# Optimization experiments

Measured on AMD Instinct MI355X. Metric: run time of the kernel, lower is better.

## Reference

```python
import jax, jax.numpy as jnp
import numpy as np

N_NODES = 100000
N_EDGES = 1600000
H, D, DE = 4, 32, 32  # heads, node_out_feats, edge_out_feats
NEG_SLOPE = 0.2


def setup_inputs() -> dict:
    key = jax.random.key(0)
    ks = jax.random.split(key, 10)
    return {
        "node_inputs": jax.random.normal(ks[0], (N_NODES, 128), jnp.float32),
        "edge_inputs": jax.random.normal(ks[1], (N_EDGES, 16), jnp.float32),
        "src": jax.random.randint(ks[2], (N_EDGES,), 0, N_NODES, jnp.int32),
        "dst": jax.random.randint(ks[3], (N_EDGES,), 0, N_NODES, jnp.int32),
        "W_fc": jax.random.normal(ks[4], (128, H * D), jnp.float32) * 0.1,
        "attn_src_p": jax.random.normal(ks[5], (1, H, D), jnp.float32) * 0.1,
        "attn_dst_p": jax.random.normal(ks[6], (1, H, D), jnp.float32) * 0.1,
        "W_edge": jax.random.normal(ks[7], (16, H * DE), jnp.float32) * 0.1,
        "attn_edge_p": jax.random.normal(ks[8], (1, H, DE), jnp.float32) * 0.1,
        "W_res": jax.random.normal(ks[9], (128, H * D), jnp.float32) * 0.1,
        "bias_p": jnp.zeros((H * D,), jnp.float32),
    }


def reference(node_inputs, edge_inputs, src, dst, W_fc, attn_src_p,
              attn_dst_p, W_edge, attn_edge_p, W_res, bias_p):
    N = node_inputs.shape[0]
    # node projection: [N, H, D]
    feat = (node_inputs @ W_fc).reshape(N, H, D)
    # per-node attention logits [N, H]
    a_src = (feat * attn_src_p).sum(-1)
    a_dst = (feat * attn_dst_p).sum(-1)
    # edge-feature attention logits [E, H]
    feat_e = (edge_inputs @ W_edge).reshape(-1, H, DE)
    a_edge = (feat_e * attn_edge_p).sum(-1)
    # per-edge score: u_add_v + edge term, then LeakyReLU
    e = a_src[src] + a_dst[dst] + a_edge                 # [E, H]
    e = jnp.where(e > 0, e, NEG_SLOPE * e)
    # edge softmax grouped by destination node
    emax = jax.lax.stop_gradient(jax.ops.segment_max(e, dst, num_segments=N))
    ex = jnp.exp(e - emax[dst])
    denom = jax.ops.segment_sum(ex, dst, num_segments=N)
    attn = ex / denom[dst]                               # [E, H]
    # weighted scatter-aggregate of source features
    msg = feat[src] * attn[:, :, None]                   # [E, H, D]
    x = jax.ops.segment_sum(msg, dst, num_segments=N)    # [N, H, D]
    # residual + bias
    x = x + (node_inputs @ W_res).reshape(N, H, D)
    x = x + bias_p.reshape(H, D)
    return x
```

## Files before the change

kernel.cpp:

```cpp
#include <hip/hip_runtime.h>
#include <math.h>

#define NNODES_FEAT 128
#define HD 128
#define H 4
#define D 32
#define EDGE_F 16
#define NEG_SLOPE 0.2f

typedef _Float16 f16;
typedef _Float16 f16x2 __attribute__((ext_vector_type(2)));
typedef _Float16 f16x4 __attribute__((ext_vector_type(4)));
typedef _Float16 f16x8 __attribute__((ext_vector_type(8)));
typedef float f32x4 __attribute__((ext_vector_type(4)));

union ExPack { float2 f; f16x4 h; };

__global__ void k_wedge(const float* __restrict__ W_edge,
                        const float* __restrict__ attn_edge,
                        float* __restrict__ w_eh) {
    int t = threadIdx.x;
    int k = t >> 2;
    int h = t & 3;
    float s = 0.f;
    for (int d = 0; d < D; ++d)
        s += W_edge[k * HD + h * D + d] * attn_edge[h * D + d];
    w_eh[k * H + h] = s;
}

__global__ __launch_bounds__(256) void k_wt(const float* __restrict__ Wfc,
                                            const float* __restrict__ Wres,
                                            f16* __restrict__ Wt) {
    int i = blockIdx.x * 256 + threadIdx.x;
    int n = i >> 7, k = i & 127;
    float v = (n < 128) ? Wfc[k * HD + n] : Wres[k * HD + (n - 128)];
    Wt[(size_t)n * 128 + k] = (f16)v;
}

#define LDK 136
__global__ __launch_bounds__(256) void k_gemm_mfma(
    const float* __restrict__ A, const f16* __restrict__ Wt,
    const float* __restrict__ bias, f16* __restrict__ feat16,
    float* __restrict__ out, int N) {
    __shared__ f16 As[64 * LDK];
    __shared__ f16 Bs[128 * LDK];
    int tid = threadIdx.x;
    int wave = tid >> 6, lane = tid & 63;
    int m0 = blockIdx.x * 64;
    int cb = blockIdx.y;

    for (int c = tid; c < 64 * 32; c += 256) {
        int r = c >> 5, cc = (c & 31) * 4;
        int gr = m0 + r;
        float4 v = make_float4(0.f, 0.f, 0.f, 0.f);
        if (gr < N) v = *(const float4*)(A + (size_t)gr * 128 + cc);
        f16x4 h = {(f16)v.x, (f16)v.y, (f16)v.z, (f16)v.w};
        *(f16x4*)(&As[r * LDK + cc]) = h;
    }
    const f16* Wblk = Wt + (size_t)cb * 128 * 128;
    for (int c = tid; c < 128 * 16; c += 256) {
        int r = c >> 4, cc = (c & 15) * 8;
        float4 v = *(const float4*)(Wblk + (size_t)r * 128 + cc);
        *(float4*)(&Bs[r * LDK + cc]) = v;
    }
    __syncthreads();

    int am = lane & 15, aq = lane >> 4;
    f32x4 acc[8];
#pragma unroll
    for (int nt = 0; nt < 8; ++nt) acc[nt] = (f32x4){0.f, 0.f, 0.f, 0.f};

    int arow = wave * 16 + am;
#pragma unroll
    for (int kc = 0; kc < 4; ++kc) {
        f16x8 a = *(const f16x8*)(&As[arow * LDK + kc * 32 + aq * 8]);
#pragma unroll
        for (int nt = 0; nt < 8; ++nt) {
            f16x8 b = *(const f16x8*)(&Bs[(nt * 16 + am) * LDK + kc * 32 + aq * 8]);
            acc[nt] = __builtin_amdgcn_mfma_f32_16x16x32_f16(a, b, acc[nt], 0, 0, 0);
        }
    }

    int orow0 = m0 + wave * 16 + aq * 4;
    if (cb == 0) {
#pragma unroll
        for (int nt = 0; nt < 8; ++nt) {
            int col = nt * 16 + am;
#pragma unroll
            for (int r = 0; r < 4; ++r) {
                int row = orow0 + r;
                if (row < N) feat16[(size_t)row * 128 + col] = (f16)acc[nt][r];
            }
        }
    } else {
#pragma unroll
        for (int nt = 0; nt < 8; ++nt) {
            int col = nt * 16 + am;
            float bv = bias[col];
#pragma unroll
            for (int r = 0; r < 4; ++r) {
                int row = orow0 + r;
                if (row < N) out[(size_t)row * 128 + col] = acc[nt][r] + bv;
            }
        }
    }
}

__global__ __launch_bounds__(256) void k_attn_nodes(
    const f16* __restrict__ feat16, const float* __restrict__ attn_src,
    const float* __restrict__ attn_dst, float* __restrict__ a_src,
    float* __restrict__ a_dst, int N) {
    int g = blockIdx.x * 256 + threadIdx.x;
    int n = g >> 2, h = g & 3;
    if (n >= N) return;
    const f16* f = feat16 + (size_t)n * HD + h * D;
    const float* w1 = attn_src + h * D;
    const float* w2 = attn_dst + h * D;
    float s1 = 0.f, s2 = 0.f;
#pragma unroll
    for (int d = 0; d < D; d += 2) {
        f16x2 fv = *(const f16x2*)(f + d);
        float f0 = (float)fv.x, f1 = (float)fv.y;
        s1 += f0 * w1[d] + f1 * w1[d + 1];
        s2 += f0 * w2[d] + f1 * w2[d + 1];
    }
    a_src[n * H + h] = s1;
    a_dst[n * H + h] = s2;
}

__global__ __launch_bounds__(256) void k_count(const int* __restrict__ dst,
                                               int* __restrict__ deg, int E) {
    int e = blockIdx.x * 256 + threadIdx.x;
    if (e < E) atomicAdd(deg + dst[e], 1);
}

__global__ __launch_bounds__(256) void k_scan_partial(
    const int* __restrict__ deg, int* __restrict__ partial, int N) {
    __shared__ int sdata[256];
    int t = threadIdx.x;
    int base = blockIdx.x * 1024 + t * 4;
    int s = 0;
#pragma unroll
    for (int j = 0; j < 4; ++j) { int i = base + j; if (i < N) s += deg[i]; }
    sdata[t] = s;
    __syncthreads();
    for (int off = 128; off > 0; off >>= 1) {
        if (t < off) sdata[t] += sdata[t + off];
        __syncthreads();
    }
    if (t == 0) partial[blockIdx.x] = sdata[0];
}

__global__ __launch_bounds__(256) void k_scan_top(
    int* __restrict__ partial, int* __restrict__ offs, int nb, int N) {
    __shared__ int sdata[256];
    int t = threadIdx.x;
    int v = (t < nb) ? partial[t] : 0;
    sdata[t] = v;
    __syncthreads();
    for (int off = 1; off < 256; off <<= 1) {
        int add = (t >= off) ? sdata[t - off] : 0;
        __syncthreads();
        sdata[t] += add;
        __syncthreads();
    }
    int excl = (t == 0) ? 0 : sdata[t - 1];
    if (t < nb) partial[t] = excl;
    if (t == nb - 1) offs[N] = sdata[t];
}

__global__ __launch_bounds__(256) void k_scan_final(
    int* __restrict__ deg_offs, const int* __restrict__ partial,
    int* __restrict__ cursor, int N) {
    __shared__ int sdata[256];
    int t = threadIdx.x;
    int base = blockIdx.x * 1024 + t * 4;
    int v[4]; int s = 0;
#pragma unroll
    for (int j = 0; j < 4; ++j) { int i = base + j; v[j] = (i < N) ? deg_offs[i] : 0; s += v[j]; }
    sdata[t] = s;
    __syncthreads();
    for (int off = 1; off < 256; off <<= 1) {
        int add = (t >= off) ? sdata[t - off] : 0;
        __syncthreads();
        sdata[t] += add;
        __syncthreads();
    }
    int excl = partial[blockIdx.x] + ((t == 0) ? 0 : sdata[t - 1]);
#pragma unroll
    for (int j = 0; j < 4; ++j) {
        int i = base + j;
        if (i < N) { deg_offs[i] = excl; cursor[i] = excl; excl += v[j]; }
    }
}

__global__ __launch_bounds__(256) void k_edge_fill(
    const float* __restrict__ edge_inputs, const int* __restrict__ src,
    const int* __restrict__ dst, const float* __restrict__ w_eh,
    const float* __restrict__ a_src, const float* __restrict__ a_dst,
    int* __restrict__ cursor, float4* __restrict__ rec, int E) {
    __shared__ float weh_s[EDGE_F * H];
    if (threadIdx.x < EDGE_F * H) weh_s[threadIdx.x] = w_eh[threadIdx.x];
    __syncthreads();

    int base = blockIdx.x * 512 + threadIdx.x;
#pragma unroll
    for (int j = 0; j < 2; ++j) {
        int e = base + j * 256;
        if (e >= E) continue;

        const float* x = edge_inputs + (long)e * EDGE_F;
        float ae[H] = {0.f, 0.f, 0.f, 0.f};
#pragma unroll
        for (int k = 0; k < EDGE_F; ++k) {
            float xv = x[k];
#pragma unroll
            for (int h = 0; h < H; ++h) ae[h] += xv * weh_s[k * H + h];
        }
        int s = src[e], d = dst[e];
        float4 as = *(const float4*)(a_src + s * H);
        float4 ad = *(const float4*)(a_dst + d * H);
        float ev[H];
        ev[0] = as.x + ad.x + ae[0];
        ev[1] = as.y + ad.y + ae[1];
        ev[2] = as.z + ad.z + ae[2];
        ev[3] = as.w + ad.w + ae[3];
#pragma unroll
        for (int h = 0; h < H; ++h) {
            float t = ev[h];
            t = t > 0.f ? t : NEG_SLOPE * t;
            ev[h] = __expf(t);
        }
        int pos = atomicAdd(cursor + d, 1);
        ExPack p;
        p.h = (f16x4){(f16)ev[0], (f16)ev[1], (f16)ev[2], (f16)ev[3]};
        float4 r;
        r.x = __int_as_float(s);
        r.y = p.f.x;
        r.z = p.f.y;
        r.w = 0.f;
        rec[pos] = r;
    }
}

__global__ __launch_bounds__(256) void k_aggr(
    const f16* __restrict__ feat16, const float4* __restrict__ rec,
    const int* __restrict__ offs, float* __restrict__ out, int N) {
    int wave = threadIdx.x >> 6;
    int lane = threadIdx.x & 63;
    int n = blockIdx.x * 4 + wave;
    if (n >= N) return;
    int beg = offs[n], end = offs[n + 1];
    if (end <= beg) return;
    int h = lane >> 4;
    size_t c0 = (size_t)2 * lane;
    float num0 = 0.f, num1 = 0.f, den = 0.f;
    int i = beg;
    for (; i + 3 < end; i += 4) {
        float4 r0 = rec[i], r1 = rec[i + 1], r2 = rec[i + 2], r3 = rec[i + 3];
        int s0 = __float_as_int(r0.x), s1 = __float_as_int(r1.x);
        int s2 = __float_as_int(r2.x), s3 = __float_as_int(r3.x);
        f16x2 f0 = *(const f16x2*)(feat16 + (size_t)s0 * HD + c0);
        f16x2 f1 = *(const f16x2*)(feat16 + (size_t)s1 * HD + c0);
        f16x2 f2 = *(const f16x2*)(feat16 + (size_t)s2 * HD + c0);
        f16x2 f3 = *(const f16x2*)(feat16 + (size_t)s3 * HD + c0);
        ExPack p0, p1, p2, p3;
        p0.f = make_float2(r0.y, r0.z);
        p1.f = make_float2(r1.y, r1.z);
        p2.f = make_float2(r2.y, r2.z);
        p3.f = make_float2(r3.y, r3.z);
        float e0 = (float)p0.h[h], e1 = (float)p1.h[h];
        float e2 = (float)p2.h[h], e3 = (float)p3.h[h];
        num0 += e0 * (float)f0.x + e1 * (float)f1.x + e2 * (float)f2.x + e3 * (float)f3.x;
        num1 += e0 * (float)f0.y + e1 * (float)f1.y + e2 * (float)f2.y + e3 * (float)f3.y;
        den += e0 + e1 + e2 + e3;
    }
    for (; i < end; ++i) {
        float4 r0 = rec[i];
        int s0 = __float_as_int(r0.x);
        f16x2 f0 = *(const f16x2*)(feat16 + (size_t)s0 * HD + c0);
        ExPack p0;
        p0.f = make_float2(r0.y, r0.z);
        float e0 = (float)p0.h[h];
        num0 += e0 * (float)f0.x;
        num1 += e0 * (float)f0.y;
        den += e0;
    }
    float inv = 1.f / den;
    size_t o = (size_t)n * HD + c0;
    float2 v = *(float2*)(out + o);
    v.x += num0 * inv;
    v.y += num1 * inv;
    *(float2*)(out + o) = v;
}

extern "C" void kernel_launch(void* const* d_in, const int* in_sizes, int n_in,
                              void* d_out, int out_size, void* d_ws, size_t ws_size,
                              hipStream_t stream) {
    const float* node_inputs = (const float*)d_in[0];
    const float* edge_inputs = (const float*)d_in[1];
    const int*   src         = (const int*)d_in[2];
    const int*   dst         = (const int*)d_in[3];
    const float* W_fc        = (const float*)d_in[4];
    const float* attn_src_p  = (const float*)d_in[5];
    const float* attn_dst_p  = (const float*)d_in[6];
    const float* W_edge      = (const float*)d_in[7];
    const float* attn_edge_p = (const float*)d_in[8];
    const float* W_res       = (const float*)d_in[9];
    const float* bias_p      = (const float*)d_in[10];

    int N = in_sizes[0] / NNODES_FEAT;
    int E = in_sizes[2];

    float* out = (float*)d_out;

    f16*    feat16  = (f16*)d_ws;
    float4* rec     = (float4*)(feat16 + (size_t)N * HD);
    f16*    Wt      = (f16*)(rec + (size_t)E);
    float*  a_src   = (float*)(Wt + 256 * 128);
    float*  a_dst   = a_src + (size_t)N * H;
    float*  w_eh    = a_dst + (size_t)N * H;
    int*    deg     = (int*)(w_eh + 64);
    int*    offs    = deg;
    int*    cursor  = deg + (N + 2);
    int*    partial = cursor + N;

    hipMemsetAsync(deg, 0, (size_t)(N + 2) * sizeof(int), stream);

    k_wedge<<<1, 64, 0, stream>>>(W_edge, attn_edge_p, w_eh);
    k_wt<<<(256 * 128) / 256, 256, 0, stream>>>(W_fc, W_res, Wt);

    dim3 g1((N + 63) / 64, 2);
    k_gemm_mfma<<<g1, 256, 0, stream>>>(node_inputs, Wt, bias_p, feat16, out, N);

    int nb = (N * H + 255) / 256;
    k_attn_nodes<<<nb, 256, 0, stream>>>(feat16, attn_src_p, attn_dst_p, a_src, a_dst, N);

    int eb = (E + 255) / 256;
    k_count<<<eb, 256, 0, stream>>>(dst, deg, E);
    int sb = (N + 1023) / 1024;
    k_scan_partial<<<sb, 256, 0, stream>>>(deg, partial, N);
    k_scan_top<<<1, 256, 0, stream>>>(partial, offs, sb, N);
    k_scan_final<<<sb, 256, 0, stream>>>(deg, partial, cursor, N);

    int eb2 = (E + 511) / 512;
    k_edge_fill<<<eb2, 256, 0, stream>>>(edge_inputs, src, dst, w_eh, a_src, a_dst,
                                         cursor, rec, E);

    int ab = (N + 3) / 4;
    k_aggr<<<ab, 256, 0, stream>>>(feat16, rec, offs, out, N);
}
```

Baseline: 516.3 us.

## Write edge records in edge order and sort via an index permutation

The edge-score kernel now writes each edge record to its original edge slot and counts degree in the same pass, which removes the separate count kernel. A new lightweight kernel scatters edge indices into CSR order using the cursors. Aggregation reads the records indirectly through this index. Record writes become coalesced, at the cost of one extra scatter pass and a random 16-byte gather per edge in aggregation.

```diff
diff --git a/kernel.cpp b/kernel.cpp
--- a/kernel.cpp
+++ b/kernel.cpp
@@ -128,77 +128,11 @@
     a_dst[n * H + h] = s2;
 }
 
-__global__ __launch_bounds__(256) void k_count(const int* __restrict__ dst,
-                                               int* __restrict__ deg, int E) {
-    int e = blockIdx.x * 256 + threadIdx.x;
-    if (e < E) atomicAdd(deg + dst[e], 1);
-}
-
-__global__ __launch_bounds__(256) void k_scan_partial(
-    const int* __restrict__ deg, int* __restrict__ partial, int N) {
-    __shared__ int sdata[256];
-    int t = threadIdx.x;
-    int base = blockIdx.x * 1024 + t * 4;
-    int s = 0;
-#pragma unroll
-    for (int j = 0; j < 4; ++j) { int i = base + j; if (i < N) s += deg[i]; }
-    sdata[t] = s;
-    __syncthreads();
-    for (int off = 128; off > 0; off >>= 1) {
-        if (t < off) sdata[t] += sdata[t + off];
-        __syncthreads();
-    }
-    if (t == 0) partial[blockIdx.x] = sdata[0];
-}
-
-__global__ __launch_bounds__(256) void k_scan_top(
-    int* __restrict__ partial, int* __restrict__ offs, int nb, int N) {
-    __shared__ int sdata[256];
-    int t = threadIdx.x;
-    int v = (t < nb) ? partial[t] : 0;
-    sdata[t] = v;
-    __syncthreads();
-    for (int off = 1; off < 256; off <<= 1) {
-        int add = (t >= off) ? sdata[t - off] : 0;
-        __syncthreads();
-        sdata[t] += add;
-        __syncthreads();
-    }
-    int excl = (t == 0) ? 0 : sdata[t - 1];
-    if (t < nb) partial[t] = excl;
-    if (t == nb - 1) offs[N] = sdata[t];
-}
-
-__global__ __launch_bounds__(256) void k_scan_final(
-    int* __restrict__ deg_offs, const int* __restrict__ partial,
-    int* __restrict__ cursor, int N) {
-    __shared__ int sdata[256];
-    int t = threadIdx.x;
-    int base = blockIdx.x * 1024 + t * 4;
-    int v[4]; int s = 0;
-#pragma unroll
-    for (int j = 0; j < 4; ++j) { int i = base + j; v[j] = (i < N) ? deg_offs[i] : 0; s += v[j]; }
-    sdata[t] = s;
-    __syncthreads();
-    for (int off = 1; off < 256; off <<= 1) {
-        int add = (t >= off) ? sdata[t - off] : 0;
-        __syncthreads();
-        sdata[t] += add;
-        __syncthreads();
-    }
-    int excl = partial[blockIdx.x] + ((t == 0) ? 0 : sdata[t - 1]);
-#pragma unroll
-    for (int j = 0; j < 4; ++j) {
-        int i = base + j;
-        if (i < N) { deg_offs[i] = excl; cursor[i] = excl; excl += v[j]; }
-    }
-}
-
-__global__ __launch_bounds__(256) void k_edge_fill(
+__global__ __launch_bounds__(256) void k_fill_count(
     const float* __restrict__ edge_inputs, const int* __restrict__ src,
     const int* __restrict__ dst, const float* __restrict__ w_eh,
     const float* __restrict__ a_src, const float* __restrict__ a_dst,
-    int* __restrict__ cursor, float4* __restrict__ rec, int E) {
+    int* __restrict__ deg, float4* __restrict__ recE, int E) {
     __shared__ float weh_s[EDGE_F * H];
     if (threadIdx.x < EDGE_F * H) weh_s[threadIdx.x] = w_eh[threadIdx.x];
     __syncthreads();
@@ -231,7 +165,6 @@
             t = t > 0.f ? t : NEG_SLOPE * t;
             ev[h] = __expf(t);
         }
-        int pos = atomicAdd(cursor + d, 1);
         ExPack p;
         p.h = (f16x4){(f16)ev[0], (f16)ev[1], (f16)ev[2], (f16)ev[3]};
         float4 r;
@@ -239,13 +172,90 @@
         r.y = p.f.x;
         r.z = p.f.y;
         r.w = 0.f;
-        rec[pos] = r;
+        recE[e] = r;
+        atomicAdd(deg + d, 1);
+    }
+}
+
+__global__ __launch_bounds__(256) void k_scan_partial(
+    const int* __restrict__ deg, int* __restrict__ partial, int N) {
+    __shared__ int sdata[256];
+    int t = threadIdx.x;
+    int base = blockIdx.x * 1024 + t * 4;
+    int s = 0;
+#pragma unroll
+    for (int j = 0; j < 4; ++j) { int i = base + j; if (i < N) s += deg[i]; }
+    sdata[t] = s;
+    __syncthreads();
+    for (int off = 128; off > 0; off >>= 1) {
+        if (t < off) sdata[t] += sdata[t + off];
+        __syncthreads();
+    }
+    if (t == 0) partial[blockIdx.x] = sdata[0];
+}
+
+__global__ __launch_bounds__(256) void k_scan_top(
+    int* __restrict__ partial, int* __restrict__ offs, int nb, int N) {
+    __shared__ int sdata[256];
+    int t = threadIdx.x;
+    int v = (t < nb) ? partial[t] : 0;
+    sdata[t] = v;
+    __syncthreads();
+    for (int off = 1; off < 256; off <<= 1) {
+        int add = (t >= off) ? sdata[t - off] : 0;
+        __syncthreads();
+        sdata[t] += add;
+        __syncthreads();
+    }
+    int excl = (t == 0) ? 0 : sdata[t - 1];
+    if (t < nb) partial[t] = excl;
+    if (t == nb - 1) offs[N] = sdata[t];
+}
+
+__global__ __launch_bounds__(256) void k_scan_final(
+    int* __restrict__ deg_offs, const int* __restrict__ partial,
+    int* __restrict__ cursor, int N) {
+    __shared__ int sdata[256];
+    int t = threadIdx.x;
+    int base = blockIdx.x * 1024 + t * 4;
+    int v[4]; int s = 0;
+#pragma unroll
+    for (int j = 0; j < 4; ++j) { int i = base + j; v[j] = (i < N) ? deg_offs[i] : 0; s += v[j]; }
+    sdata[t] = s;
+    __syncthreads();
+    for (int off = 1; off < 256; off <<= 1) {
+        int add = (t >= off) ? sdata[t - off] : 0;
+        __syncthreads();
+        sdata[t] += add;
+        __syncthreads();
+    }
+    int excl = partial[blockIdx.x] + ((t == 0) ? 0 : sdata[t - 1]);
+#pragma unroll
+    for (int j = 0; j < 4; ++j) {
+        int i = base + j;
+        if (i < N) { deg_offs[i] = excl; cursor[i] = excl; excl += v[j]; }
+    }
+}
+
+__global__ __launch_bounds__(256) void k_perm(
+    const int* __restrict__ dst, int* __restrict__ cursor,
+    int* __restrict__ eidx, int E) {
+    int base = blockIdx.x * 2048 + threadIdx.x;
+#pragma unroll
+    for (int j = 0; j < 8; ++j) {
+        int e = base + j * 256;
+        if (e < E) {
+            int d = dst[e];
+            int pos = atomicAdd(cursor + d, 1);
+            eidx[pos] = e;
+        }
     }
 }
 
 __global__ __launch_bounds__(256) void k_aggr(
-    const f16* __restrict__ feat16, const float4* __restrict__ rec,
-    const int* __restrict__ offs, float* __restrict__ out, int N) {
+    const f16* __restrict__ feat16, const float4* __restrict__ recE,
+    const int* __restrict__ eidx, const int* __restrict__ offs,
+    float* __restrict__ out, int N) {
     int wave = threadIdx.x >> 6;
     int lane = threadIdx.x & 63;
     int n = blockIdx.x * 4 + wave;
@@ -257,7 +267,8 @@
     float num0 = 0.f, num1 = 0.f, den = 0.f;
     int i = beg;
     for (; i + 3 < end; i += 4) {
-        float4 r0 = rec[i], r1 = rec[i + 1], r2 = rec[i + 2], r3 = rec[i + 3];
+        int e0 = eidx[i], e1 = eidx[i + 1], e2 = eidx[i + 2], e3 = eidx[i + 3];
+        float4 r0 = recE[e0], r1 = recE[e1], r2 = recE[e2], r3 = recE[e3];
         int s0 = __float_as_int(r0.x), s1 = __float_as_int(r1.x);
         int s2 = __float_as_int(r2.x), s3 = __float_as_int(r3.x);
         f16x2 f0 = *(const f16x2*)(feat16 + (size_t)s0 * HD + c0);
@@ -269,22 +280,23 @@
         p1.f = make_float2(r1.y, r1.z);
         p2.f = make_float2(r2.y, r2.z);
         p3.f = make_float2(r3.y, r3.z);
-        float e0 = (float)p0.h[h], e1 = (float)p1.h[h];
-        float e2 = (float)p2.h[h], e3 = (float)p3.h[h];
-        num0 += e0 * (float)f0.x + e1 * (float)f1.x + e2 * (float)f2.x + e3 * (float)f3.x;
-        num1 += e0 * (float)f0.y + e1 * (float)f1.y + e2 * (float)f2.y + e3 * (float)f3.y;
-        den += e0 + e1 + e2 + e3;
+        float e0v = (float)p0.h[h], e1v = (float)p1.h[h];
+        float e2v = (float)p2.h[h], e3v = (float)p3.h[h];
+        num0 += e0v * (float)f0.x + e1v * (float)f1.x + e2v * (float)f2.x + e3v * (float)f3.x;
+        num1 += e0v * (float)f0.y + e1v * (float)f1.y + e2v * (float)f2.y + e3v * (float)f3.y;
+        den += e0v + e1v + e2v + e3v;
     }
     for (; i < end; ++i) {
-        float4 r0 = rec[i];
+        int e0 = eidx[i];
+        float4 r0 = recE[e0];
         int s0 = __float_as_int(r0.x);
         f16x2 f0 = *(const f16x2*)(feat16 + (size_t)s0 * HD + c0);
         ExPack p0;
         p0.f = make_float2(r0.y, r0.z);
-        float e0 = (float)p0.h[h];
-        num0 += e0 * (float)f0.x;
-        num1 += e0 * (float)f0.y;
-        den += e0;
+        float e0v = (float)p0.h[h];
+        num0 += e0v * (float)f0.x;
+        num1 += e0v * (float)f0.y;
+        den += e0v;
     }
     float inv = 1.f / den;
     size_t o = (size_t)n * HD + c0;
@@ -315,8 +327,9 @@
     float* out = (float*)d_out;
 
     f16*    feat16  = (f16*)d_ws;
-    float4* rec     = (float4*)(feat16 + (size_t)N * HD);
-    f16*    Wt      = (f16*)(rec + (size_t)E);
+    float4* recE    = (float4*)(feat16 + (size_t)N * HD);
+    int*    eidx    = (int*)(recE + (size_t)E);
+    f16*    Wt      = (f16*)(eidx + (size_t)E);
     float*  a_src   = (float*)(Wt + 256 * 128);
     float*  a_dst   = a_src + (size_t)N * H;
     float*  w_eh    = a_dst + (size_t)N * H;
@@ -336,17 +349,18 @@
     int nb = (N * H + 255) / 256;
     k_attn_nodes<<<nb, 256, 0, stream>>>(feat16, attn_src_p, attn_dst_p, a_src, a_dst, N);
 
-    int eb = (E + 255) / 256;
-    k_count<<<eb, 256, 0, stream>>>(dst, deg, E);
+    int eb2 = (E + 511) / 512;
+    k_fill_count<<<eb2, 256, 0, stream>>>(edge_inputs, src, dst, w_eh, a_src, a_dst,
+                                          deg, recE, E);
+
     int sb = (N + 1023) / 1024;
     k_scan_partial<<<sb, 256, 0, stream>>>(deg, partial, N);
     k_scan_top<<<1, 256, 0, stream>>>(partial, offs, sb, N);
     k_scan_final<<<sb, 256, 0, stream>>>(deg, partial, cursor, N);
 
-    int eb2 = (E + 511) / 512;
-    k_edge_fill<<<eb2, 256, 0, stream>>>(edge_inputs, src, dst, w_eh, a_src, a_dst,
-                                         cursor, rec, E);
+    int pb = (E + 2047) / 2048;
+    k_perm<<<pb, 256, 0, stream>>>(dst, cursor, eidx, E);
 
     int ab = (N + 3) / 4;
-    k_aggr<<<ab, 256, 0, stream>>>(feat16, rec, offs, out, N);
-}
+    k_aggr<<<ab, 256, 0, stream>>>(feat16, recE, eidx, offs, out, N);
+}
```

After: 603.4 us. 1.17x slower.

## Replace global-atomic CSR scatter with two-level bucketed partition sort

Applied to the files above, without the earlier changes.

Edge scores are now written in original edge order, and degree counting is fused into that fill kernel along with a per-bucket histogram. A coarse pass partitions edge indices into 196 destination buckets, and a fine pass per bucket scatters records into CSR order using shared-memory cursors. This replaces random global atomicAdd cursors and scattered 16-byte writes with more local writes. The cost is extra passes, a 16-byte-per-edge record buffer and an index buffer, plus bucket-count constants that assume N is at most 196*512.

```diff
diff --git a/kernel.cpp b/kernel.cpp
--- a/kernel.cpp
+++ b/kernel.cpp
@@ -7,6 +7,10 @@
 #define D 32
 #define EDGE_F 16
 #define NEG_SLOPE 0.2f
+
+#define CB_SHIFT 9
+#define NBUCK 196
+#define BH_STRIDE 16
 
 typedef _Float16 f16;
 typedef _Float16 f16x2 __attribute__((ext_vector_type(2)));
@@ -128,79 +132,16 @@
     a_dst[n * H + h] = s2;
 }
 
-__global__ __launch_bounds__(256) void k_count(const int* __restrict__ dst,
-                                               int* __restrict__ deg, int E) {
-    int e = blockIdx.x * 256 + threadIdx.x;
-    if (e < E) atomicAdd(deg + dst[e], 1);
-}
-
-__global__ __launch_bounds__(256) void k_scan_partial(
-    const int* __restrict__ deg, int* __restrict__ partial, int N) {
-    __shared__ int sdata[256];
-    int t = threadIdx.x;
-    int base = blockIdx.x * 1024 + t * 4;
-    int s = 0;
-#pragma unroll
-    for (int j = 0; j < 4; ++j) { int i = base + j; if (i < N) s += deg[i]; }
-    sdata[t] = s;
-    __syncthreads();
-    for (int off = 128; off > 0; off >>= 1) {
-        if (t < off) sdata[t] += sdata[t + off];
-        __syncthreads();
-    }
-    if (t == 0) partial[blockIdx.x] = sdata[0];
-}
-
-__global__ __launch_bounds__(256) void k_scan_top(
-    int* __restrict__ partial, int* __restrict__ offs, int nb, int N) {
-    __shared__ int sdata[256];
-    int t = threadIdx.x;
-    int v = (t < nb) ? partial[t] : 0;
-    sdata[t] = v;
-    __syncthreads();
-    for (int off = 1; off < 256; off <<= 1) {
-        int add = (t >= off) ? sdata[t - off] : 0;
-        __syncthreads();
-        sdata[t] += add;
-        __syncthreads();
-    }
-    int excl = (t == 0) ? 0 : sdata[t - 1];
-    if (t < nb) partial[t] = excl;
-    if (t == nb - 1) offs[N] = sdata[t];
-}
-
-__global__ __launch_bounds__(256) void k_scan_final(
-    int* __restrict__ deg_offs, const int* __restrict__ partial,
-    int* __restrict__ cursor, int N) {
-    __shared__ int sdata[256];
-    int t = threadIdx.x;
-    int base = blockIdx.x * 1024 + t * 4;
-    int v[4]; int s = 0;
-#pragma unroll
-    for (int j = 0; j < 4; ++j) { int i = base + j; v[j] = (i < N) ? deg_offs[i] : 0; s += v[j]; }
-    sdata[t] = s;
-    __syncthreads();
-    for (int off = 1; off < 256; off <<= 1) {
-        int add = (t >= off) ? sdata[t - off] : 0;
-        __syncthreads();
-        sdata[t] += add;
-        __syncthreads();
-    }
-    int excl = partial[blockIdx.x] + ((t == 0) ? 0 : sdata[t - 1]);
-#pragma unroll
-    for (int j = 0; j < 4; ++j) {
-        int i = base + j;
-        if (i < N) { deg_offs[i] = excl; cursor[i] = excl; excl += v[j]; }
-    }
-}
-
-__global__ __launch_bounds__(256) void k_edge_fill(
+__global__ __launch_bounds__(256) void k_fill_count(
     const float* __restrict__ edge_inputs, const int* __restrict__ src,
     const int* __restrict__ dst, const float* __restrict__ w_eh,
     const float* __restrict__ a_src, const float* __restrict__ a_dst,
-    int* __restrict__ cursor, float4* __restrict__ rec, int E) {
+    int* __restrict__ deg, int* __restrict__ bhist,
+    float4* __restrict__ recE, int E) {
     __shared__ float weh_s[EDGE_F * H];
+    __shared__ int hist[NBUCK];
     if (threadIdx.x < EDGE_F * H) weh_s[threadIdx.x] = w_eh[threadIdx.x];
+    if (threadIdx.x < NBUCK) hist[threadIdx.x] = 0;
     __syncthreads();
 
     int base = blockIdx.x * 512 + threadIdx.x;
@@ -231,7 +172,6 @@
             t = t > 0.f ? t : NEG_SLOPE * t;
             ev[h] = __expf(t);
         }
-        int pos = atomicAdd(cursor + d, 1);
         ExPack p;
         p.h = (f16x4){(f16)ev[0], (f16)ev[1], (f16)ev[2], (f16)ev[3]};
         float4 r;
@@ -239,7 +179,145 @@
         r.y = p.f.x;
         r.z = p.f.y;
         r.w = 0.f;
-        rec[pos] = r;
+        recE[e] = r;
+        atomicAdd(deg + d, 1);
+        atomicAdd(&hist[d >> CB_SHIFT], 1);
+    }
+    __syncthreads();
+    if (threadIdx.x < NBUCK && hist[threadIdx.x] > 0)
+        atomicAdd(bhist + threadIdx.x * BH_STRIDE, hist[threadIdx.x]);
+}
+
+__global__ __launch_bounds__(256) void k_scan_partial(
+    const int* __restrict__ deg, int* __restrict__ partial, int N) {
+    __shared__ int sdata[256];
+    int t = threadIdx.x;
+    int base = blockIdx.x * 1024 + t * 4;
+    int s = 0;
+#pragma unroll
+    for (int j = 0; j < 4; ++j) { int i = base + j; if (i < N) s += deg[i]; }
+    sdata[t] = s;
+    __syncthreads();
+    for (int off = 128; off > 0; off >>= 1) {
+        if (t < off) sdata[t] += sdata[t + off];
+        __syncthreads();
+    }
+    if (t == 0) partial[blockIdx.x] = sdata[0];
+}
+
+__global__ __launch_bounds__(256) void k_scan_top(
+    int* __restrict__ partial, int* __restrict__ offs, int nb, int N) {
+    __shared__ int sdata[256];
+    int t = threadIdx.x;
+    int v = (t < nb) ? partial[t] : 0;
+    sdata[t] = v;
+    __syncthreads();
+    for (int off = 1; off < 256; off <<= 1) {
+        int add = (t >= off) ? sdata[t - off] : 0;
+        __syncthreads();
+        sdata[t] += add;
+        __syncthreads();
+    }
+    int excl = (t == 0) ? 0 : sdata[t - 1];
+    if (t < nb) partial[t] = excl;
+    if (t == nb - 1) offs[N] = sdata[t];
+}
+
+__global__ __launch_bounds__(256) void k_scan_final(
+    int* __restrict__ deg_offs, const int* __restrict__ partial, int N) {
+    __shared__ int sdata[256];
+    int t = threadIdx.x;
+    int base = blockIdx.x * 1024 + t * 4;
+    int v[4]; int s = 0;
+#pragma unroll
+    for (int j = 0; j < 4; ++j) { int i = base + j; v[j] = (i < N) ? deg_offs[i] : 0; s += v[j]; }
+    sdata[t] = s;
+    __syncthreads();
+    for (int off = 1; off < 256; off <<= 1) {
+        int add = (t >= off) ? sdata[t - off] : 0;
+        __syncthreads();
+        sdata[t] += add;
+        __syncthreads();
+    }
+    int excl = partial[blockIdx.x] + ((t == 0) ? 0 : sdata[t - 1]);
+#pragma unroll
+    for (int j = 0; j < 4; ++j) {
+        int i = base + j;
+        if (i < N) { deg_offs[i] = excl; excl += v[j]; }
+    }
+}
+
+__global__ __launch_bounds__(256) void k_bscan(
+    const int* __restrict__ bhist, int* __restrict__ bbase,
+    int* __restrict__ gcur) {
+    __shared__ int sdata[256];
+    int t = threadIdx.x;
+    int v = (t < NBUCK) ? bhist[t * BH_STRIDE] : 0;
+    sdata[t] = v;
+    __syncthreads();
+    for (int off = 1; off < 256; off <<= 1) {
+        int add = (t >= off) ? sdata[t - off] : 0;
+        __syncthreads();
+        sdata[t] += add;
+        __syncthreads();
+    }
+    int excl = (t == 0) ? 0 : sdata[t - 1];
+    if (t < NBUCK) {
+        bbase[t] = excl;
+        gcur[t * BH_STRIDE] = excl;
+    }
+    if (t == NBUCK - 1) bbase[NBUCK] = sdata[t];
+}
+
+__global__ __launch_bounds__(256) void k_part_coarse(
+    const int* __restrict__ dst, int* __restrict__ gcur,
+    int* __restrict__ ebuck, int E) {
+    __shared__ int hist[NBUCK];
+    __shared__ int curl[NBUCK];
+    int t = threadIdx.x;
+    if (t < NBUCK) hist[t] = 0;
+    __syncthreads();
+
+    int base = blockIdx.x * 4096;
+#pragma unroll
+    for (int j = 0; j < 16; ++j) {
+        int e = base + j * 256 + t;
+        if (e < E) atomicAdd(&hist[dst[e] >> CB_SHIFT], 1);
+    }
+    __syncthreads();
+    if (t < NBUCK && hist[t] > 0)
+        curl[t] = atomicAdd(&gcur[t * BH_STRIDE], hist[t]);
+    __syncthreads();
+#pragma unroll
+    for (int j = 0; j < 16; ++j) {
+        int e = base + j * 256 + t;
+        if (e < E) {
+            int b = dst[e] >> CB_SHIFT;
+            int pos = atomicAdd(&curl[b], 1);
+            ebuck[pos] = e;
+        }
+    }
+}
+
+__global__ __launch_bounds__(1024) void k_part_fine(
+    const int* __restrict__ dst, const int* __restrict__ ebuck,
+    const int* __restrict__ bbase, const int* __restrict__ offs,
+    const float4* __restrict__ recE, float4* __restrict__ rec_sorted, int N) {
+    __shared__ int cur[1 << CB_SHIFT];
+    int t = threadIdx.x;
+    int b = blockIdx.x;
+    int dbase = b << CB_SHIFT;
+    if (t < (1 << CB_SHIFT)) {
+        int idx = dbase + t;
+        cur[t] = offs[idx < N ? idx : N];
+    }
+    __syncthreads();
+    int beg = bbase[b], end = bbase[b + 1];
+    for (int i = beg + t; i < end; i += 1024) {
+        int e = ebuck[i];
+        int d = dst[e];
+        int pos = atomicAdd(&cur[d - dbase], 1);
+        rec_sorted[pos] = recE[e];
     }
 }
 
@@ -314,18 +392,22 @@
 
     float* out = (float*)d_out;
 
-    f16*    feat16  = (f16*)d_ws;
-    float4* rec     = (float4*)(feat16 + (size_t)N * HD);
-    f16*    Wt      = (f16*)(rec + (size_t)E);
-    float*  a_src   = (float*)(Wt + 256 * 128);
-    float*  a_dst   = a_src + (size_t)N * H;
-    float*  w_eh    = a_dst + (size_t)N * H;
-    int*    deg     = (int*)(w_eh + 64);
-    int*    offs    = deg;
-    int*    cursor  = deg + (N + 2);
-    int*    partial = cursor + N;
-
-    hipMemsetAsync(deg, 0, (size_t)(N + 2) * sizeof(int), stream);
+    f16*    feat16     = (f16*)d_ws;
+    float4* recE       = (float4*)(feat16 + (size_t)N * HD);
+    float4* rec_sorted = recE + (size_t)E;
+    int*    ebuck      = (int*)(rec_sorted + (size_t)E);
+    f16*    Wt         = (f16*)(ebuck + (size_t)E);
+    float*  a_src      = (float*)(Wt + 256 * 128);
+    float*  a_dst      = a_src + (size_t)N * H;
+    float*  w_eh       = a_dst + (size_t)N * H;
+    int*    deg        = (int*)(w_eh + 64);
+    int*    offs       = deg;
+    int*    bhist      = deg + (N + 2);
+    int*    gcur       = bhist + NBUCK * BH_STRIDE;
+    int*    bbase      = gcur + NBUCK * BH_STRIDE;
+    int*    partial    = bbase + (NBUCK + 4);
+
+    hipMemsetAsync(deg, 0, (size_t)(N + 2 + NBUCK * BH_STRIDE) * sizeof(int), stream);
 
     k_wedge<<<1, 64, 0, stream>>>(W_edge, attn_edge_p, w_eh);
     k_wt<<<(256 * 128) / 256, 256, 0, stream>>>(W_fc, W_res, Wt);
@@ -336,17 +418,21 @@
     int nb = (N * H + 255) / 256;
     k_attn_nodes<<<nb, 256, 0, stream>>>(feat16, attn_src_p, attn_dst_p, a_src, a_dst, N);
 
-    int eb = (E + 255) / 256;
-    k_count<<<eb, 256, 0, stream>>>(dst, deg, E);
+    int eb2 = (E + 511) / 512;
+    k_fill_count<<<eb2, 256, 0, stream>>>(edge_inputs, src, dst, w_eh, a_src, a_dst,
+                                          deg, bhist, recE, E);
+
     int sb = (N + 1023) / 1024;
     k_scan_partial<<<sb, 256, 0, stream>>>(deg, partial, N);
     k_scan_top<<<1, 256, 0, stream>>>(partial, offs, sb, N);
-    k_scan_final<<<sb, 256, 0, stream>>>(deg, partial, cursor, N);
-
-    int eb2 = (E + 511) / 512;
-    k_edge_fill<<<eb2, 256, 0, stream>>>(edge_inputs, src, dst, w_eh, a_src, a_dst,
-                                         cursor, rec, E);
+    k_scan_final<<<sb, 256, 0, stream>>>(deg, partial, N);
+
+    k_bscan<<<1, 256, 0, stream>>>(bhist, bbase, gcur);
+
+    int cb = (E + 4095) / 4096;
+    k_part_coarse<<<cb, 256, 0, stream>>>(dst, gcur, ebuck, E);
+    k_part_fine<<<NBUCK, 1024, 0, stream>>>(dst, ebuck, bbase, offs, recE, rec_sorted, N);
 
     int ab = (N + 3) / 4;
-    k_aggr<<<ab, 256, 0, stream>>>(feat16, rec, offs, out, N);
-}
+    k_aggr<<<ab, 256, 0, stream>>>(feat16, rec_sorted, offs, out, N);
+}
```

New measurement: 561.6 us. 8.8% more time.
